# Optimization experiments

Hardware: AMD Instinct MI355X
Metric: run time of the kernel (lower is better)

Reference implementation:

```python
import jax, jax.numpy as jnp
import numpy as np

DIM = 1024
DFF = 4096
LN_EPS = 1e-5


def _layernorm(x, g, b):
    mu = jnp.mean(x, axis=-1, keepdims=True)
    var = jnp.mean((x - mu) ** 2, axis=-1, keepdims=True)
    return (x - mu) * jax.lax.rsqrt(var + LN_EPS) * g + b


def setup_inputs() -> dict:
    key = jax.random.key(0)
    ks = jax.random.split(key, 16)
    B, L, D, F = 4, 2048, DIM, DFF
    return {
        "x": jax.random.normal(ks[0], (B, L, D), dtype=jnp.float32),
        "hidden_real": jax.random.normal(ks[1], (B, D), dtype=jnp.float32),
        "hidden_imag": jax.random.normal(ks[2], (B, D), dtype=jnp.float32),
        # SConvLayer params (real/imag pairs, mirroring torch.view_as_real storage)
        "phazor_init": jax.random.normal(ks[3], (D, 2), dtype=jnp.float32),
        "phazor": jax.random.normal(ks[4], (D, 2), dtype=jnp.float32),
        # fc (gate) linear
        "fc_w": jax.random.normal(ks[5], (D, D), dtype=jnp.float32) / np.sqrt(D),
        "fc_b": jax.random.normal(ks[6], (D,), dtype=jnp.float32) * 0.01,
        # FFN
        "w1": jax.random.normal(ks[7], (F, D), dtype=jnp.float32) / np.sqrt(D),
        "b1": jax.random.normal(ks[8], (F,), dtype=jnp.float32) * 0.01,
        "w2": jax.random.normal(ks[9], (D, F), dtype=jnp.float32) / np.sqrt(F),
        "b2": jax.random.normal(ks[10], (D,), dtype=jnp.float32) * 0.01,
        # shared LayerNorm (used twice in the block with the same params)
        "ln_g": jnp.ones((D,), dtype=jnp.float32),
        "ln_b": jnp.zeros((D,), dtype=jnp.float32),
    }


def reference(x, hidden_real, hidden_imag, phazor_init, phazor,
              fc_w, fc_b, w1, b1, w2, b2, ln_g, ln_b):
    B, L, D = x.shape
    hidden = (hidden_real + 1j * hidden_imag).astype(jnp.complex64)

    x_res = x
    xn = _layernorm(x, ln_g, ln_b)

    # --- SConvLayer ---
    pz = (phazor[:, 0] + 1j * phazor[:, 1]).astype(jnp.complex64)  # [D]
    # magnitude exp(-|z|^2), phase = angle(z)
    p = jnp.exp(-(pz.real ** 2 + pz.imag ** 2)) * jnp.exp(1j * jnp.angle(pz))
    t = jnp.arange(L)
    prog = p[None, :] ** t[:, None]                      # [L, D] complex
    init_c = (phazor_init[:, 0] + 1j * phazor_init[:, 1]).astype(jnp.complex64)
    filt = prog * init_c[None, :]                        # [L, D]
    n2 = 2 * L
    filt_fft = jnp.fft.fft(filt, n=n2, axis=0)           # [2L, D]
    x_fft = jnp.fft.fft(xn.astype(jnp.complex64), n=n2, axis=1)  # [B, 2L, D]
    conv = jnp.fft.ifft(filt_fft[None] * x_fft, axis=1)[:, :L]   # [B, L, D]
    conv_with_past = conv + hidden[:, None, :] * prog[None] * p[None, None, :]
    sx = conv_with_past.real

    # --- gate ---
    y = jax.nn.silu(jnp.einsum('bld,ed->ble', x_res, fc_w) + fc_b)
    x2 = sx * y + x_res

    # --- FFN (same LayerNorm params) ---
    x3 = _layernorm(x2, ln_g, ln_b)
    h = jax.nn.silu(jnp.einsum('bld,fd->blf', x3, w1) + b1)
    out = jnp.einsum('blf,df->bld', h, w2) + b2 + x2
    return out, conv_with_past
```

## Files before the change

### kernel.cpp

```cpp
#include <hip/hip_runtime.h>
#include <hip/hip_bf16.h>

#define D_MODEL 1024
#define D_FF    4096
#define SEQ_LEN 2048
#define NBATCH  4
#define NROWS   (NBATCH*SEQ_LEN)
#define NCHUNK  32
#define CHUNK_L (SEQ_LEN/NCHUNK)
#define LN_EPS  1e-5f

typedef __hip_bfloat16 bf16;
typedef __attribute__((ext_vector_type(8))) short bf16x8;
typedef __attribute__((ext_vector_type(4))) float f32x4;

__device__ __forceinline__ void gload16(const bf16* g, bf16* l) {
    __builtin_amdgcn_global_load_lds(
        (const __attribute__((address_space(1))) void*)g,
        (__attribute__((address_space(3))) void*)l, 16, 0, 0);
}

__global__ void cast4(const float4* __restrict__ in, ushort4* __restrict__ out, int n4) {
    int i = blockIdx.x * blockDim.x + threadIdx.x;
    if (i < n4) {
        float4 v = in[i];
        union { ushort4 u; bf16 b[4]; } cv;
        cv.b[0] = __float2bfloat16(v.x); cv.b[1] = __float2bfloat16(v.y);
        cv.b[2] = __float2bfloat16(v.z); cv.b[3] = __float2bfloat16(v.w);
        out[i] = cv.u;
    }
}

__global__ void compute_pvec(const float* __restrict__ phz, float* __restrict__ pv) {
    int d = blockIdx.x * blockDim.x + threadIdx.x;
    if (d >= D_MODEL) return;
    float re = phz[2*d], im = phz[2*d+1];
    float r2 = re*re + im*im;
    float mag = expf(-r2);
    float pr, pim;
    if (r2 > 0.f) { float inv = mag / sqrtf(r2); pr = re*inv; pim = im*inv; }
    else          { pr = mag; pim = 0.f; }
    float ar = pr, ai = pim;
    #pragma unroll
    for (int i = 0; i < 6; i++) { float nr = ar*ar - ai*ai; float ni = 2.f*ar*ai; ar = nr; ai = ni; }
    pv[d]            = pr;
    pv[D_MODEL+d]    = pim;
    pv[2*D_MODEL+d]  = ar;
    pv[3*D_MODEL+d]  = ai;
}

__global__ __launch_bounds__(256) void ln_fused(const float* __restrict__ x,
                                                const float* __restrict__ g,
                                                const float* __restrict__ bta,
                                                float* __restrict__ outf,
                                                bf16*  __restrict__ outb,
                                                bf16*  __restrict__ rawb)
{
    int row = blockIdx.x;
    int tid = threadIdx.x;
    const float4* xr = (const float4*)(x + (size_t)row * D_MODEL);
    float4 v = xr[tid];
    if (rawb) {
        union { ushort4 u; bf16 b[4]; } cv;
        cv.b[0]=__float2bfloat16(v.x); cv.b[1]=__float2bfloat16(v.y);
        cv.b[2]=__float2bfloat16(v.z); cv.b[3]=__float2bfloat16(v.w);
        ((ushort4*)(rawb + (size_t)row * D_MODEL))[tid] = cv.u;
    }
    float s  = v.x + v.y + v.z + v.w;
    float s2 = v.x*v.x + v.y*v.y + v.z*v.z + v.w*v.w;
    for (int off = 32; off; off >>= 1) { s += __shfl_down(s, off); s2 += __shfl_down(s2, off); }
    __shared__ float red[8];
    int wid = tid >> 6, lane = tid & 63;
    if (lane == 0) { red[wid] = s; red[4+wid] = s2; }
    __syncthreads();
    if (tid == 0) {
        red[0] = red[0]+red[1]+red[2]+red[3];
        red[4] = red[4]+red[5]+red[6]+red[7];
    }
    __syncthreads();
    float mu  = red[0] * (1.f/D_MODEL);
    float var = red[4] * (1.f/D_MODEL) - mu*mu;
    float rstd = rsqrtf(var + LN_EPS);
    float4 gv = ((const float4*)g)[tid];
    float4 bv = ((const float4*)bta)[tid];
    float4 o;
    o.x = (v.x-mu)*rstd*gv.x + bv.x;
    o.y = (v.y-mu)*rstd*gv.y + bv.y;
    o.z = (v.z-mu)*rstd*gv.z + bv.z;
    o.w = (v.w-mu)*rstd*gv.w + bv.w;
    if (outf) ((float4*)(outf + (size_t)row * D_MODEL))[tid] = o;
    if (outb) {
        union { ushort4 u; bf16 b[4]; } cv;
        cv.b[0]=__float2bfloat16(o.x); cv.b[1]=__float2bfloat16(o.y);
        cv.b[2]=__float2bfloat16(o.z); cv.b[3]=__float2bfloat16(o.w);
        ((ushort4*)(outb + (size_t)row * D_MODEL))[tid] = cv.u;
    }
}

__global__ __launch_bounds__(256) void scan_pass1(const float* __restrict__ xn,
                                                  const float* __restrict__ pv,
                                                  const float* __restrict__ pini,
                                                  float* __restrict__ Sc)
{
    int d = blockIdx.x * 256 + threadIdx.x;
    int c = blockIdx.y, b = blockIdx.z;
    float pr = pv[d], pim = pv[D_MODEL+d];
    float icr = pini[2*d], ici = pini[2*d+1];
    float Sr = 0.f, Si = 0.f;
    const float* xp = xn + ((size_t)b*SEQ_LEN + c*CHUNK_L) * D_MODEL + d;
    #pragma unroll 8
    for (int i = 0; i < CHUNK_L; i++) {
        float xv = xp[(size_t)i * D_MODEL];
        float nr = pr*Sr - pim*Si + icr*xv;
        float ni = pr*Si + pim*Sr + ici*xv;
        Sr = nr; Si = ni;
    }
    size_t o = ((size_t)b*NCHUNK + c) * D_MODEL + d;
    Sc[2*o] = Sr; Sc[2*o+1] = Si;
}

__global__ __launch_bounds__(256) void scan_prefix(const float* __restrict__ Sc,
                                                   const float* __restrict__ pv,
                                                   const float* __restrict__ hr,
                                                   const float* __restrict__ hi,
                                                   float* __restrict__ pref)
{
    int d = blockIdx.x * 256 + threadIdx.x;
    int b = blockIdx.y;
    float qr = pv[2*D_MODEL+d], qi = pv[3*D_MODEL+d];
    float Ur = hr[b*D_MODEL+d], Ui = hi[b*D_MODEL+d];
    for (int c = 0; c < NCHUNK; c++) {
        size_t o = ((size_t)b*NCHUNK + c) * D_MODEL + d;
        pref[2*o] = Ur; pref[2*o+1] = Ui;
        float sr = Sc[2*o], si = Sc[2*o+1];
        float nr = qr*Ur - qi*Ui + sr;
        float ni = qr*Ui + qi*Ur + si;
        Ur = nr; Ui = ni;
    }
}

__global__ __launch_bounds__(256) void scan_pass2(const float* __restrict__ xn,
                                                  const float* __restrict__ pv,
                                                  const float* __restrict__ pini,
                                                  const float* __restrict__ pref,
                                                  float* __restrict__ cwp,
                                                  int interleaved)
{
    int d = blockIdx.x * 256 + threadIdx.x;
    int c = blockIdx.y, b = blockIdx.z;
    float pr = pv[d], pim = pv[D_MODEL+d];
    float icr = pini[2*d], ici = pini[2*d+1];
    size_t po = ((size_t)b*NCHUNK + c) * D_MODEL + d;
    float Ur = pref[2*po], Ui = pref[2*po+1];
    size_t base = ((size_t)b*SEQ_LEN + c*CHUNK_L) * D_MODEL + d;
    const float* xp = xn + base;
    if (interleaved) {
        float2* cp = (float2*)cwp + base;
        #pragma unroll 8
        for (int i = 0; i < CHUNK_L; i++) {
            float xv = xp[(size_t)i * D_MODEL];
            float nr = pr*Ur - pim*Ui + icr*xv;
            float ni = pr*Ui + pim*Ur + ici*xv;
            Ur = nr; Ui = ni;
            cp[(size_t)i * D_MODEL] = make_float2(Ur, Ui);
        }
    } else {
        float* cp = cwp + base;
        #pragma unroll 8
        for (int i = 0; i < CHUNK_L; i++) {
            float xv = xp[(size_t)i * D_MODEL];
            float nr = pr*Ur - pim*Ui + icr*xv;
            float ni = pr*Ui + pim*Ur + ici*xv;
            Ur = nr; Ui = ni;
            cp[(size_t)i * D_MODEL] = Ur;
        }
    }
}

template<int EPI>
__device__ __forceinline__ void epi_store(float v, size_t idx,
                                          const float* e0, int e0_stride, const float* e1,
                                          float* outf, bf16* outb)
{
    if (EPI == 0) {
        float yv = v / (1.f + __expf(-v));
        float sxv = e0[idx * (size_t)e0_stride];
        outf[idx] = sxv * yv + e1[idx];
    } else if (EPI == 1) {
        float yv = v / (1.f + __expf(-v));
        outb[idx] = __float2bfloat16(yv);
    } else {
        outf[idx] = v + e0[idx];
    }
}

#define BM 128
#define BN 128
#define BK 32

template<int EPI>
__global__ __launch_bounds__(256) void gemm_bt(const bf16* __restrict__ A,
                                               const bf16* __restrict__ Bt,
                                               const float* __restrict__ bias,
                                               const float* __restrict__ e0, int e0_stride,
                                               const float* __restrict__ e1,
                                               float* __restrict__ outf,
                                               bf16*  __restrict__ outb,
                                               int M, int N, int K)
{
    __shared__ __align__(16) bf16 As[3][BM*BK];
    __shared__ __align__(16) bf16 Bs[3][BM*BK];
    int tid = threadIdx.x;
    int m0 = blockIdx.x * BM;
    int n0 = blockIdx.y * BN;

    int wid = tid >> 6, lane = tid & 63;
    int wm = (wid >> 1) * 64, wn = (wid & 1) * 64;
    int lr = lane & 15;
    int lkc = lane >> 4;

    int rl = lane >> 2;
    int cS = (lane & 3) ^ ((rl >> 1) & 3);
    const bf16* gA0 = A  + (size_t)(m0 +      wid*16 + rl) * K + cS*8;
    const bf16* gA1 = A  + (size_t)(m0 + 64 + wid*16 + rl) * K + cS*8;
    const bf16* gB0 = Bt + (size_t)(n0 +      wid*16 + rl) * K + cS*8;
    const bf16* gB1 = Bt + (size_t)(n0 + 64 + wid*16 + rl) * K + cS*8;
    int lo0 = (     wid*16) * BK;
    int lo1 = (64 + wid*16) * BK;

    int keyr = (lr >> 1) & 3;
    int cR = (lkc ^ keyr) * 8;
    int offA[4], offB[4];
    #pragma unroll
    for (int i = 0; i < 4; i++) {
        offA[i] = (wm + i*16 + lr) * BK + cR;
        offB[i] = (wn + i*16 + lr) * BK + cR;
    }

    int nt = K / BK;
    auto stage = [&](int slot, int tile) {
        int k0 = tile * BK;
        gload16(gA0 + k0, &As[slot][lo0]);
        gload16(gA1 + k0, &As[slot][lo1]);
        gload16(gB0 + k0, &Bs[slot][lo0]);
        gload16(gB1 + k0, &Bs[slot][lo1]);
    };
    f32x4 acc[4][4] = {};
    auto compute = [&](int slot) {
        bf16x8 af[4], bfv[4];
        #pragma unroll
        for (int i = 0; i < 4; i++) {
            af[i]  = *(const bf16x8*)&As[slot][offA[i]];
            bfv[i] = *(const bf16x8*)&Bs[slot][offB[i]];
        }
        #pragma unroll
        for (int i = 0; i < 4; i++)
            #pragma unroll
            for (int j = 0; j < 4; j++)
                acc[i][j] = __builtin_amdgcn_mfma_f32_16x16x32_bf16(af[i], bfv[j], acc[i][j], 0, 0, 0);
    };

    stage(0, 0); stage(1, 1); stage(2, 2);

    int s = 0;
    for (int t = 0; t < nt - 3; ++t) {
        asm volatile("s_waitcnt vmcnt(8)" ::: "memory");
        __builtin_amdgcn_s_barrier();
        __builtin_amdgcn_sched_barrier(0);
        compute(s);
        asm volatile("" ::: "memory");
        __builtin_amdgcn_s_barrier();
        stage(s, t + 3);
        s = (s == 2) ? 0 : s + 1;
    }
    asm volatile("s_waitcnt vmcnt(8)" ::: "memory");
    __builtin_amdgcn_s_barrier();
    __builtin_amdgcn_sched_barrier(0);
    compute(s);
    s = (s == 2) ? 0 : s + 1;
    asm volatile("s_waitcnt vmcnt(4)" ::: "memory");
    __builtin_amdgcn_s_barrier();
    __builtin_amdgcn_sched_barrier(0);
    compute(s);
    s = (s == 2) ? 0 : s + 1;
    asm volatile("s_waitcnt vmcnt(0)" ::: "memory");
    __builtin_amdgcn_s_barrier();
    __builtin_amdgcn_sched_barrier(0);
    compute(s);

    int mrow = 4 * (lane >> 4);
    #pragma unroll
    for (int i = 0; i < 4; i++) {
        #pragma unroll
        for (int j = 0; j < 4; j++) {
            int nb = n0 + wn + j*16 + lr;
            float bb = bias[nb];
            #pragma unroll
            for (int r = 0; r < 4; r++) {
                int m = m0 + wm + i*16 + mrow + r;
                size_t idx = (size_t)m * N + nb;
                epi_store<EPI>(acc[i][j][r] + bb, idx, e0, e0_stride, e1, outf, outb);
            }
        }
    }
}

#define TM 256
#define TN 256

template<int EPI>
__global__ __launch_bounds__(512, 2) void gemm256(const bf16* __restrict__ A,
                                                  const bf16* __restrict__ Bt,
                                                  const float* __restrict__ bias,
                                                  const float* __restrict__ e0, int e0_stride,
                                                  const float* __restrict__ e1,
                                                  float* __restrict__ outf,
                                                  bf16*  __restrict__ outb,
                                                  int M, int N, int K)
{
    __shared__ __align__(16) bf16 As[3][TM*BK];
    __shared__ __align__(16) bf16 Bs[3][TN*BK];
    int tid = threadIdx.x;
    int m0 = blockIdx.x * TM;
    int n0 = blockIdx.y * TN;

    int wid = tid >> 6, lane = tid & 63;
    int wr = wid >> 2, wc = wid & 3;
    int wm = wr * 128, wn = wc * 64;
    int lr = lane & 15;
    int lkc = lane >> 4;

    int rl = tid >> 2;
    int cS = (tid & 3) ^ ((rl >> 1) & 3);
    const bf16* gA0 = A  + (size_t)(m0 +       rl) * K + cS*8;
    const bf16* gA1 = A  + (size_t)(m0 + 128 + rl) * K + cS*8;
    const bf16* gB0 = Bt + (size_t)(n0 +       rl) * K + cS*8;
    const bf16* gB1 = Bt + (size_t)(n0 + 128 + rl) * K + cS*8;
    int lo0 = (      wid*16) * BK;
    int lo1 = (128 + wid*16) * BK;

    int keyr = (lr >> 1) & 3;
    int cR = (lkc ^ keyr) * 8;
    int offA[8], offB[4];
    #pragma unroll
    for (int i = 0; i < 8; i++) offA[i] = (wm + i*16 + lr) * BK + cR;
    #pragma unroll
    for (int j = 0; j < 4; j++) offB[j] = (wn + j*16 + lr) * BK + cR;

    int nt = K / BK;
    auto stage = [&](int slot, int tile) {
        int k0 = tile * BK;
        gload16(gA0 + k0, &As[slot][lo0]);
        gload16(gA1 + k0, &As[slot][lo1]);
        gload16(gB0 + k0, &Bs[slot][lo0]);
        gload16(gB1 + k0, &Bs[slot][lo1]);
    };
    f32x4 acc[8][4] = {};
    auto compute = [&](int slot) {
        bf16x8 af[8], bfv[4];
        #pragma unroll
        for (int i = 0; i < 8; i++) af[i]  = *(const bf16x8*)&As[slot][offA[i]];
        #pragma unroll
        for (int j = 0; j < 4; j++) bfv[j] = *(const bf16x8*)&Bs[slot][offB[j]];
        #pragma unroll
        for (int i = 0; i < 8; i++)
            #pragma unroll
            for (int j = 0; j < 4; j++)
                acc[i][j] = __builtin_amdgcn_mfma_f32_16x16x32_bf16(af[i], bfv[j], acc[i][j], 0, 0, 0);
    };

    stage(0, 0); stage(1, 1); stage(2, 2);

    int s = 0;
    for (int t = 0; t < nt - 3; ++t) {
        asm volatile("s_waitcnt vmcnt(8)" ::: "memory");
        __builtin_amdgcn_s_barrier();
        __builtin_amdgcn_sched_barrier(0);
        compute(s);
        asm volatile("" ::: "memory");
        __builtin_amdgcn_s_barrier();
        stage(s, t + 3);
        s = (s == 2) ? 0 : s + 1;
    }
    asm volatile("s_waitcnt vmcnt(8)" ::: "memory");
    __builtin_amdgcn_s_barrier();
    __builtin_amdgcn_sched_barrier(0);
    compute(s);
    s = (s == 2) ? 0 : s + 1;
    asm volatile("s_waitcnt vmcnt(4)" ::: "memory");
    __builtin_amdgcn_s_barrier();
    __builtin_amdgcn_sched_barrier(0);
    compute(s);
    s = (s == 2) ? 0 : s + 1;
    asm volatile("s_waitcnt vmcnt(0)" ::: "memory");
    __builtin_amdgcn_s_barrier();
    __builtin_amdgcn_sched_barrier(0);
    compute(s);

    int mrow = 4 * (lane >> 4);
    #pragma unroll
    for (int i = 0; i < 8; i++) {
        #pragma unroll
        for (int j = 0; j < 4; j++) {
            int nb = n0 + wn + j*16 + lr;
            float bb = bias[nb];
            #pragma unroll
            for (int r = 0; r < 4; r++) {
                int m = m0 + wm + i*16 + mrow + r;
                size_t idx = (size_t)m * N + nb;
                epi_store<EPI>(acc[i][j][r] + bb, idx, e0, e0_stride, e1, outf, outb);
            }
        }
    }
}

extern "C" void kernel_launch(void* const* d_in, const int* in_sizes, int n_in,
                              void* d_out, int out_size, void* d_ws, size_t ws_size,
                              hipStream_t stream)
{
    const float* x    = (const float*)d_in[0];
    const float* hr   = (const float*)d_in[1];
    const float* hi   = (const float*)d_in[2];
    const float* pini = (const float*)d_in[3];
    const float* phz  = (const float*)d_in[4];
    const float* fcw  = (const float*)d_in[5];
    const float* fcb  = (const float*)d_in[6];
    const float* w1   = (const float*)d_in[7];
    const float* b1   = (const float*)d_in[8];
    const float* w2   = (const float*)d_in[9];
    const float* b2   = (const float*)d_in[10];
    const float* lng  = (const float*)d_in[11];
    const float* lnb  = (const float*)d_in[12];

    float* out = (float*)d_out;
    float* cwp = out + (size_t)NROWS * D_MODEL;
    int interleaved = (out_size >= NROWS * D_MODEL * 3) ? 1 : 0;

    char* ws = (char*)d_ws;
    size_t off = 0;
    bf16*  wfcb = (bf16*)(ws + off);  off += (size_t)D_MODEL*D_MODEL*2;
    bf16*  w1b  = (bf16*)(ws + off);  off += (size_t)D_FF*D_MODEL*2;
    bf16*  w2b  = (bf16*)(ws + off);  off += (size_t)D_MODEL*D_FF*2;
    float* pv   = (float*)(ws + off); off += (size_t)4*D_MODEL*4;
    float* xn   = (float*)(ws + off); off += (size_t)NROWS*D_MODEL*4;
    bf16*  xbf  = (bf16*)(ws + off);  off += (size_t)NROWS*D_MODEL*2;
    float* Sc   = (float*)(ws + off); off += (size_t)NBATCH*NCHUNK*D_MODEL*2*4;
    float* pref = (float*)(ws + off); off += (size_t)NBATCH*NCHUNK*D_MODEL*2*4;
    float* x2   = (float*)(ws + off); off += (size_t)NROWS*D_MODEL*4;
    bf16*  x3b  = (bf16*)(ws + off);  off += (size_t)NROWS*D_MODEL*2;
    bf16*  hbuf = (bf16*)(ws + off);  off += (size_t)NROWS*D_FF*2;

    cast4<<<1024, 256, 0, stream>>>((const float4*)fcw, (ushort4*)wfcb, D_MODEL*D_MODEL/4);
    cast4<<<4096, 256, 0, stream>>>((const float4*)w1,  (ushort4*)w1b,  D_FF*D_MODEL/4);
    cast4<<<4096, 256, 0, stream>>>((const float4*)w2,  (ushort4*)w2b,  D_MODEL*D_FF/4);

    compute_pvec<<<4, 256, 0, stream>>>(phz, pv);

    ln_fused<<<NROWS, 256, 0, stream>>>(x, lng, lnb, xn, nullptr, xbf);

    scan_pass1<<<dim3(4, NCHUNK, NBATCH), 256, 0, stream>>>(xn, pv, pini, Sc);
    scan_prefix<<<dim3(4, NBATCH), 256, 0, stream>>>(Sc, pv, hr, hi, pref);
    scan_pass2<<<dim3(4, NCHUNK, NBATCH), 256, 0, stream>>>(xn, pv, pini, pref, cwp, interleaved);

    gemm_bt<0><<<dim3(NROWS/BM, D_MODEL/BN), 256, 0, stream>>>(
        xbf, wfcb, fcb, cwp, interleaved ? 2 : 1, x, x2, nullptr, NROWS, D_MODEL, D_MODEL);

    ln_fused<<<NROWS, 256, 0, stream>>>(x2, lng, lnb, nullptr, x3b, nullptr);

    gemm256<1><<<dim3(NROWS/TM, D_FF/TN), 512, 0, stream>>>(
        x3b, w1b, b1, nullptr, 1, nullptr, nullptr, hbuf, NROWS, D_FF, D_MODEL);

    gemm_bt<2><<<dim3(NROWS/BM, D_MODEL/BN), 256, 0, stream>>>(
        hbuf, w2b, b2, x2, 1, nullptr, out, nullptr, NROWS, D_MODEL, D_FF);
}
```

Before: 271.8 us.

## Move gate combine into LayerNorm kernel and double-buffer the FFN1 GEMM

The gate GEMM now writes only the bf16 SiLU output. A new gate_ln kernel combines it with the convolution output and the residual, writes x2 and computes the second LayerNorm in one row pass. This replaces the GEMM epilogue's strided scattered reads and the separate LN kernel, at the cost of an extra bf16 intermediate buffer and bf16 rounding of the gate value. Separately, gemm256 drops from triple to double buffering in LDS, with the launch-bounds occupancy hint raised to 4, trading prefetch depth for more resident blocks.

New measurement: 655.5 us. 2.41x slower.

```diff
diff --git a/kernel.cpp b/kernel.cpp
--- a/kernel.cpp
+++ b/kernel.cpp
@@ -95,6 +95,59 @@
         cv.b[2]=__float2bfloat16(o.z); cv.b[3]=__float2bfloat16(o.w);
         ((ushort4*)(outb + (size_t)row * D_MODEL))[tid] = cv.u;
     }
+}
+
+__global__ __launch_bounds__(256) void gate_ln(const float* __restrict__ cwp, int cstride,
+                                               const bf16*  __restrict__ y,
+                                               const float* __restrict__ x,
+                                               const float* __restrict__ g,
+                                               const float* __restrict__ bta,
+                                               float* __restrict__ x2,
+                                               bf16*  __restrict__ x3b)
+{
+    int row = blockIdx.x;
+    int tid = threadIdx.x;
+    size_t base = (size_t)row * D_MODEL + tid*4;
+    float4 xv = *(const float4*)(x + base);
+    union { ushort4 u; bf16 b[4]; } yv;
+    yv.u = *(const ushort4*)(y + base);
+    float4 cw;
+    if (cstride == 1) {
+        cw = *(const float4*)(cwp + base);
+    } else {
+        const float2* cp = (const float2*)cwp + base;
+        cw.x = cp[0].x; cw.y = cp[1].x; cw.z = cp[2].x; cw.w = cp[3].x;
+    }
+    float4 v;
+    v.x = cw.x * __bfloat162float(yv.b[0]) + xv.x;
+    v.y = cw.y * __bfloat162float(yv.b[1]) + xv.y;
+    v.z = cw.z * __bfloat162float(yv.b[2]) + xv.z;
+    v.w = cw.w * __bfloat162float(yv.b[3]) + xv.w;
+    *(float4*)(x2 + base) = v;
+
+    float s  = v.x + v.y + v.z + v.w;
+    float s2 = v.x*v.x + v.y*v.y + v.z*v.z + v.w*v.w;
+    for (int off = 32; off; off >>= 1) { s += __shfl_down(s, off); s2 += __shfl_down(s2, off); }
+    __shared__ float red[8];
+    int wid = tid >> 6, lane = tid & 63;
+    if (lane == 0) { red[wid] = s; red[4+wid] = s2; }
+    __syncthreads();
+    if (tid == 0) {
+        red[0] = red[0]+red[1]+red[2]+red[3];
+        red[4] = red[4]+red[5]+red[6]+red[7];
+    }
+    __syncthreads();
+    float mu  = red[0] * (1.f/D_MODEL);
+    float var = red[4] * (1.f/D_MODEL) - mu*mu;
+    float rstd = rsqrtf(var + LN_EPS);
+    float4 gv = ((const float4*)g)[tid];
+    float4 bv = ((const float4*)bta)[tid];
+    union { ushort4 u; bf16 b[4]; } cv;
+    cv.b[0] = __float2bfloat16((v.x-mu)*rstd*gv.x + bv.x);
+    cv.b[1] = __float2bfloat16((v.y-mu)*rstd*gv.y + bv.y);
+    cv.b[2] = __float2bfloat16((v.z-mu)*rstd*gv.z + bv.z);
+    cv.b[3] = __float2bfloat16((v.w-mu)*rstd*gv.w + bv.w);
+    *(ushort4*)(x3b + base) = cv.u;
 }
 
 __global__ __launch_bounds__(256) void scan_pass1(const float* __restrict__ xn,
@@ -182,11 +235,7 @@
                                           const float* e0, int e0_stride, const float* e1,
                                           float* outf, bf16* outb)
 {
-    if (EPI == 0) {
-        float yv = v / (1.f + __expf(-v));
-        float sxv = e0[idx * (size_t)e0_stride];
-        outf[idx] = sxv * yv + e1[idx];
-    } else if (EPI == 1) {
+    if (EPI == 1) {
         float yv = v / (1.f + __expf(-v));
         outb[idx] = __float2bfloat16(yv);
     } else {
@@ -309,7 +358,7 @@
 #define TN 256
 
 template<int EPI>
-__global__ __launch_bounds__(512, 2) void gemm256(const bf16* __restrict__ A,
+__global__ __launch_bounds__(512, 4) void gemm256(const bf16* __restrict__ A,
                                                   const bf16* __restrict__ Bt,
                                                   const float* __restrict__ bias,
                                                   const float* __restrict__ e0, int e0_stride,
@@ -318,8 +367,8 @@
                                                   bf16*  __restrict__ outb,
                                                   int M, int N, int K)
 {
-    __shared__ __align__(16) bf16 As[3][TM*BK];
-    __shared__ __align__(16) bf16 Bs[3][TN*BK];
+    __shared__ __align__(16) bf16 As[2][TM*BK];
+    __shared__ __align__(16) bf16 Bs[2][TN*BK];
     int tid = threadIdx.x;
     int m0 = blockIdx.x * TM;
     int n0 = blockIdx.y * TN;
@@ -369,29 +418,24 @@
                 acc[i][j] = __builtin_amdgcn_mfma_f32_16x16x32_bf16(af[i], bfv[j], acc[i][j], 0, 0, 0);
     };
 
-    stage(0, 0); stage(1, 1); stage(2, 2);
+    stage(0, 0); stage(1, 1);
 
     int s = 0;
-    for (int t = 0; t < nt - 3; ++t) {
-        asm volatile("s_waitcnt vmcnt(8)" ::: "memory");
+    for (int t = 0; t < nt - 2; ++t) {
+        asm volatile("s_waitcnt vmcnt(4)" ::: "memory");
         __builtin_amdgcn_s_barrier();
         __builtin_amdgcn_sched_barrier(0);
         compute(s);
         asm volatile("" ::: "memory");
         __builtin_amdgcn_s_barrier();
-        stage(s, t + 3);
-        s = (s == 2) ? 0 : s + 1;
-    }
-    asm volatile("s_waitcnt vmcnt(8)" ::: "memory");
-    __builtin_amdgcn_s_barrier();
-    __builtin_amdgcn_sched_barrier(0);
-    compute(s);
-    s = (s == 2) ? 0 : s + 1;
+        stage(s, t + 2);
+        s ^= 1;
+    }
     asm volatile("s_waitcnt vmcnt(4)" ::: "memory");
     __builtin_amdgcn_s_barrier();
     __builtin_amdgcn_sched_barrier(0);
     compute(s);
-    s = (s == 2) ? 0 : s + 1;
+    s ^= 1;
     asm volatile("s_waitcnt vmcnt(0)" ::: "memory");
     __builtin_amdgcn_s_barrier();
     __builtin_amdgcn_sched_barrier(0);
@@ -449,6 +493,7 @@
     float* x2   = (float*)(ws + off); off += (size_t)NROWS*D_MODEL*4;
     bf16*  x3b  = (bf16*)(ws + off);  off += (size_t)NROWS*D_MODEL*2;
     bf16*  hbuf = (bf16*)(ws + off);  off += (size_t)NROWS*D_FF*2;
+    bf16*  ybuf = (bf16*)(ws + off);  off += (size_t)NROWS*D_MODEL*2;
 
     cast4<<<1024, 256, 0, stream>>>((const float4*)fcw, (ushort4*)wfcb, D_MODEL*D_MODEL/4);
     cast4<<<4096, 256, 0, stream>>>((const float4*)w1,  (ushort4*)w1b,  D_FF*D_MODEL/4);
@@ -462,10 +507,10 @@
     scan_prefix<<<dim3(4, NBATCH), 256, 0, stream>>>(Sc, pv, hr, hi, pref);
     scan_pass2<<<dim3(4, NCHUNK, NBATCH), 256, 0, stream>>>(xn, pv, pini, pref, cwp, interleaved);
 
-    gemm_bt<0><<<dim3(NROWS/BM, D_MODEL/BN), 256, 0, stream>>>(
-        xbf, wfcb, fcb, cwp, interleaved ? 2 : 1, x, x2, nullptr, NROWS, D_MODEL, D_MODEL);
-
-    ln_fused<<<NROWS, 256, 0, stream>>>(x2, lng, lnb, nullptr, x3b, nullptr);
+    gemm_bt<1><<<dim3(NROWS/BM, D_MODEL/BN), 256, 0, stream>>>(
+        xbf, wfcb, fcb, nullptr, 1, nullptr, nullptr, ybuf, NROWS, D_MODEL, D_MODEL);
+
+    gate_ln<<<NROWS, 256, 0, stream>>>(cwp, interleaved ? 2 : 1, ybuf, x, lng, lnb, x2, x3b);
 
     gemm256<1><<<dim3(NROWS/TM, D_FF/TN), 512, 0, stream>>>(
         x3b, w1b, b1, nullptr, 1, nullptr, nullptr, hbuf, NROWS, D_FF, D_MODEL);
```
